# Kernel tuning notes

Hardware: AMD Instinct MI355X
Metric: run time of the kernel (lower is better)

The kernel has to match this reference:

```python
import jax, jax.numpy as jnp
import numpy as np

T = 5          # Newton iterations (init kwarg T)
EPS = 1e-05    # covariance regularizer (init kwarg eps)


def setup_inputs() -> dict:
    key = jax.random.key(0)
    k1, k2 = jax.random.split(key)
    B, C, H, W = 64, 128, 56, 56
    x = jax.random.normal(k1, (B, C, H, W), dtype=jnp.float32)
    running_rot = jax.random.normal(k2, (C, C), dtype=jnp.float32)
    return {"x": x, "running_rot": running_rot}


def reference(x, running_rot):
    # Concept Whitening forward (training-mode batch statistics), channels_first.
    # 1) IterNorm ZCA whitening via T Newton iterations on the CxC covariance.
    # 2) Rotation by the (non-trainable) running rotation matrix.
    B, C, H, W = x.shape
    m = B * H * W
    # (C, m): channels as rows, all samples/locations as columns
    xt = x.transpose(1, 0, 2, 3).reshape(C, m)
    mean = jnp.mean(xt, axis=1, keepdims=True)
    xc = xt - mean
    I = jnp.eye(C, dtype=x.dtype)
    Sigma = EPS * I + (xc @ xc.T) / m            # (C, C)
    rTr = 1.0 / jnp.trace(Sigma)                 # trace normalization
    SigmaN = Sigma * rTr
    P = I
    for _ in range(T):                           # Newton iteration for Sigma^{-1/2}
        P = 0.5 * (3.0 * P - P @ P @ P @ SigmaN)
    wm = P * jnp.sqrt(rTr)                       # whitening matrix Sigma^{-1/2}
    xn = wm @ xc                                 # whitened activations (C, m)
    x_hat = xn.reshape(C, B, H, W).transpose(1, 0, 2, 3)  # (B, C, H, W)
    # rotate into concept-aligned basis: out[b,d,h,w] = sum_c rot[d,c] * x_hat[b,c,h,w]
    out = jnp.einsum('bchw,dc->bdhw', x_hat, running_rot)
    return out
```

## Files before the change

kernel.cpp:

```cpp
#include <hip/hip_runtime.h>
#include <math.h>

#define HW 3136
#define NCHUNK 3136
#define M_TOT 200704.0f
#define EPSV 1e-5f

typedef __attribute__((ext_vector_type(8))) short bf16x8;
typedef __attribute__((ext_vector_type(4))) short short4v;
typedef __attribute__((ext_vector_type(4))) float f32x4;

__device__ inline unsigned short f2bf(float f) {
  unsigned u = __float_as_uint(f);
  u += 0x7FFFu + ((u >> 16) & 1u);
  return (unsigned short)(u >> 16);
}

__global__ __launch_bounds__(256, 2) void gram_k(const float* __restrict__ x,
                                                 float* __restrict__ partG,
                                                 float* __restrict__ partS,
                                                 int slots) {
  __shared__ unsigned short xs[128 * 72];
  const int t = threadIdx.x;
  const int lm = t & 15, quad = (t >> 4) & 3, w = t >> 6;

  f32x4 acc[2][8];
  f32x4 sacc[2];
  const f32x4 z = {0.f, 0.f, 0.f, 0.f};
#pragma unroll
  for (int i = 0; i < 2; ++i) {
    sacc[i] = z;
#pragma unroll
    for (int j = 0; j < 8; ++j) acc[i][j] = z;
  }
  bf16x8 ones;
#pragma unroll
  for (int j = 0; j < 8; ++j) ones[j] = (short)0x3F80;

  for (int chunk = blockIdx.x; chunk < NCHUNK; chunk += slots) {
    const int b = chunk / 49;
    const int s0 = (chunk % 49) * 64;
    __syncthreads();
#pragma unroll
    for (int i = 0; i < 8; ++i) {
      const int idx4 = i * 256 + t;
      const int c = idx4 >> 4, q = idx4 & 15;
      const float4 v =
          *(const float4*)(x + (size_t)(b * 128 + c) * HW + s0 + q * 4);
      uint2 dw;
      dw.x = (unsigned)f2bf(v.x) | ((unsigned)f2bf(v.y) << 16);
      dw.y = (unsigned)f2bf(v.z) | ((unsigned)f2bf(v.w) << 16);
      *(uint2*)&xs[c * 72 + q * 4] = dw;
    }
    __syncthreads();
#pragma unroll
    for (int ks = 0; ks < 2; ++ks) {
      const int ko = ks * 32 + quad * 8;
      const bf16x8 a0 = *(const bf16x8*)&xs[((2 * w + 0) * 16 + lm) * 72 + ko];
      const bf16x8 a1 = *(const bf16x8*)&xs[((2 * w + 1) * 16 + lm) * 72 + ko];
      sacc[0] = __builtin_amdgcn_mfma_f32_16x16x32_bf16(a0, ones, sacc[0], 0, 0, 0);
      sacc[1] = __builtin_amdgcn_mfma_f32_16x16x32_bf16(a1, ones, sacc[1], 0, 0, 0);
#pragma unroll
      for (int tj = 0; tj < 8; ++tj) {
        const bf16x8 bf = *(const bf16x8*)&xs[(tj * 16 + lm) * 72 + ko];
        acc[0][tj] = __builtin_amdgcn_mfma_f32_16x16x32_bf16(a0, bf, acc[0][tj], 0, 0, 0);
        acc[1][tj] = __builtin_amdgcn_mfma_f32_16x16x32_bf16(a1, bf, acc[1][tj], 0, 0, 0);
      }
    }
  }

  float* pg = partG + (size_t)blockIdx.x * 16384;
#pragma unroll
  for (int i = 0; i < 2; ++i) {
    const int ti = 2 * w + i;
#pragma unroll
    for (int tj = 0; tj < 8; ++tj)
#pragma unroll
      for (int r = 0; r < 4; ++r)
        pg[(ti * 16 + quad * 4 + r) * 128 + tj * 16 + lm] = acc[i][tj][r];
    if (lm == 0) {
#pragma unroll
      for (int r = 0; r < 4; ++r)
        partS[blockIdx.x * 128 + ti * 16 + quad * 4 + r] = sacc[i][r];
    }
  }
}

__global__ __launch_bounds__(256) void reduce1_k(const float* __restrict__ partG,
                                                 const float* __restrict__ partS,
                                                 float* __restrict__ part2,
                                                 float* __restrict__ part2S,
                                                 int slots) {
  const int t = threadIdx.x;
  const int sg = blockIdx.x & 31;
  const int eg = blockIdx.x >> 5;
  const int e4 = eg * 1024 + t * 4;
  float ax = 0.f, ay = 0.f, az = 0.f, aw = 0.f;
#pragma unroll 4
  for (int s = sg; s < slots; s += 32) {
    const float4 v = *(const float4*)(partG + (size_t)s * 16384 + e4);
    ax += v.x; ay += v.y; az += v.z; aw += v.w;
  }
  *(float4*)(part2 + (size_t)sg * 16384 + e4) = make_float4(ax, ay, az, aw);
  if (eg == 0 && t < 128) {
    float sa = 0.f;
    for (int s = sg; s < slots; s += 32) sa += partS[s * 128 + t];
    part2S[sg * 128 + t] = sa;
  }
}

__global__ __launch_bounds__(256) void reduce2_k(const float* __restrict__ part2,
                                                 const float* __restrict__ part2S,
                                                 float* __restrict__ G,
                                                 float* __restrict__ Sb) {
  const int t = threadIdx.x;
  const int e4 = blockIdx.x * 1024 + t * 4;
  float ax = 0.f, ay = 0.f, az = 0.f, aw = 0.f;
#pragma unroll
  for (int sg = 0; sg < 32; ++sg) {
    const float4 v = *(const float4*)(part2 + (size_t)sg * 16384 + e4);
    ax += v.x; ay += v.y; az += v.z; aw += v.w;
  }
  *(float4*)(G + e4) = make_float4(ax, ay, az, aw);
  if (blockIdx.x == 0 && t < 128) {
    float sa = 0.f;
#pragma unroll
    for (int sg = 0; sg < 32; ++sg) sa += part2S[sg * 128 + t];
    Sb[t] = sa;
  }
}

__global__ __launch_bounds__(256) void sigma_k(const float* __restrict__ G,
                                               float* __restrict__ Sb,
                                               float* __restrict__ SigmaN,
                                               float* __restrict__ Pa,
                                               float* __restrict__ scal) {
  const int t = threadIdx.x;
  const float rm = 1.0f / M_TOT;
  float trl = 0.f;
#pragma unroll 4
  for (int i = 0; i < 64; ++i) {
    const int e = i * 256 + t;
    const int r = e >> 7, c = e & 127;
    float v = (G[e] - Sb[r] * Sb[c] * rm) * rm + ((r == c) ? EPSV : 0.f);
    SigmaN[e] = v;
    if (r == c) trl += v;
  }
  __shared__ float red[256];
  red[t] = trl;
  __syncthreads();
  for (int off = 128; off > 0; off >>= 1) {
    if (t < off) red[t] += red[t + off];
    __syncthreads();
  }
  const float rTr = 1.0f / red[0];
#pragma unroll 4
  for (int i = 0; i < 64; ++i) {
    const int e = i * 256 + t;
    const int r = e >> 7, c = e & 127;
    const float sn = SigmaN[e] * rTr;
    SigmaN[e] = sn;
    Pa[e] = ((r == c) ? 1.5f : 0.f) - 0.5f * sn;
  }
  if (t < 128) Sb[t] *= rm;
  if (t == 0) scal[0] = sqrtf(rTr);
}

__global__ __launch_bounds__(256) void newton_k(const float* __restrict__ P,
                                                const float* __restrict__ SigmaN,
                                                float* __restrict__ Pout) {
  __shared__ float s1[8 * 132];
  __shared__ float s2[8 * 132];
  __shared__ float red[256 * 17];
  const int t = threadIdx.x;
  const int ct = t & 31;
  const int rt = (t >> 5) & 1;
  const int kt = t >> 6;
  const int rg0 = blockIdx.x * 8;
  float a[4][4];

#pragma unroll
  for (int i = 0; i < 4; ++i)
#pragma unroll
    for (int j = 0; j < 4; ++j) a[i][j] = 0.f;
#pragma unroll 4
  for (int k = kt * 32; k < kt * 32 + 32; ++k) {
    const float4 av = *(const float4*)(P + k * 128 + rg0 + 4 * rt);
    const float4 bv = *(const float4*)(P + k * 128 + 4 * ct);
    const float aA[4] = {av.x, av.y, av.z, av.w};
    const float bA[4] = {bv.x, bv.y, bv.z, bv.w};
#pragma unroll
    for (int i = 0; i < 4; ++i)
#pragma unroll
      for (int j = 0; j < 4; ++j) a[i][j] += aA[i] * bA[j];
  }
#pragma unroll
  for (int i = 0; i < 4; ++i)
#pragma unroll
    for (int j = 0; j < 4; ++j) red[t * 17 + i * 4 + j] = a[i][j];
  __syncthreads();
  if (t < 64) {
#pragma unroll
    for (int u = 1; u < 4; ++u)
#pragma unroll
      for (int i = 0; i < 4; ++i)
#pragma unroll
        for (int j = 0; j < 4; ++j)
          a[i][j] += red[(t + 64 * u) * 17 + i * 4 + j];
#pragma unroll
    for (int i = 0; i < 4; ++i)
#pragma unroll
      for (int j = 0; j < 4; ++j)
        s1[(4 * rt + i) * 132 + 4 * ct + j] = a[i][j];
  }
  __syncthreads();

#pragma unroll
  for (int i = 0; i < 4; ++i)
#pragma unroll
    for (int j = 0; j < 4; ++j) a[i][j] = 0.f;
#pragma unroll 4
  for (int k = kt * 32; k < kt * 32 + 32; ++k) {
    float aA[4];
#pragma unroll
    for (int i = 0; i < 4; ++i) aA[i] = s1[(4 * rt + i) * 132 + k];
    const float4 bv = *(const float4*)(P + k * 128 + 4 * ct);
    const float bA[4] = {bv.x, bv.y, bv.z, bv.w};
#pragma unroll
    for (int i = 0; i < 4; ++i)
#pragma unroll
      for (int j = 0; j < 4; ++j) a[i][j] += aA[i] * bA[j];
  }
  __syncthreads();
#pragma unroll
  for (int i = 0; i < 4; ++i)
#pragma unroll
    for (int j = 0; j < 4; ++j) red[t * 17 + i * 4 + j] = a[i][j];
  __syncthreads();
  if (t < 64) {
#pragma unroll
    for (int u = 1; u < 4; ++u)
#pragma unroll
      for (int i = 0; i < 4; ++i)
#pragma unroll
        for (int j = 0; j < 4; ++j)
          a[i][j] += red[(t + 64 * u) * 17 + i * 4 + j];
#pragma unroll
    for (int i = 0; i < 4; ++i)
#pragma unroll
      for (int j = 0; j < 4; ++j)
        s2[(4 * rt + i) * 132 + 4 * ct + j] = a[i][j];
  }
  __syncthreads();

#pragma unroll
  for (int i = 0; i < 4; ++i)
#pragma unroll
    for (int j = 0; j < 4; ++j) a[i][j] = 0.f;
#pragma unroll 4
  for (int k = kt * 32; k < kt * 32 + 32; ++k) {
    float aA[4];
#pragma unroll
    for (int i = 0; i < 4; ++i) aA[i] = s2[(4 * rt + i) * 132 + k];
    const float4 bv = *(const float4*)(SigmaN + k * 128 + 4 * ct);
    const float bA[4] = {bv.x, bv.y, bv.z, bv.w};
#pragma unroll
    for (int i = 0; i < 4; ++i)
#pragma unroll
      for (int j = 0; j < 4; ++j) a[i][j] += aA[i] * bA[j];
  }
  __syncthreads();
#pragma unroll
  for (int i = 0; i < 4; ++i)
#pragma unroll
    for (int j = 0; j < 4; ++j) red[t * 17 + i * 4 + j] = a[i][j];
  __syncthreads();
  if (t < 64) {
#pragma unroll
    for (int u = 1; u < 4; ++u)
#pragma unroll
      for (int i = 0; i < 4; ++i)
#pragma unroll
        for (int j = 0; j < 4; ++j)
          a[i][j] += red[(t + 64 * u) * 17 + i * 4 + j];
#pragma unroll
    for (int i = 0; i < 4; ++i) {
      const int rg = rg0 + 4 * rt + i;
      const float4 pv = *(const float4*)(P + rg * 128 + 4 * ct);
      *(float4*)(Pout + rg * 128 + 4 * ct) =
          make_float4(0.5f * (3.f * pv.x - a[i][0]),
                      0.5f * (3.f * pv.y - a[i][1]),
                      0.5f * (3.f * pv.z - a[i][2]),
                      0.5f * (3.f * pv.w - a[i][3]));
    }
  }
}

__global__ __launch_bounds__(256) void rotmt_k(const float* __restrict__ rot,
                                               const float* __restrict__ P,
                                               const float* __restrict__ mean,
                                               const float* __restrict__ scal,
                                               unsigned short* __restrict__ Mbf,
                                               float* __restrict__ bias) {
  const int t = threadIdx.x;
  const int r = t >> 5;
  const int dg = blockIdx.x * 8 + r;
  const int c0 = (t & 31) * 4;
  const float* rrow = rot + dg * 128;

  float ax = 0, ay = 0, az = 0, aw = 0;
#pragma unroll 4
  for (int k = 0; k < 128; ++k) {
    const float a = rrow[k];
    const float4 bv = *(const float4*)(P + k * 128 + c0);
    ax += a * bv.x; ay += a * bv.y; az += a * bv.z; aw += a * bv.w;
  }
  const float sc = scal[0];
  ax *= sc; ay *= sc; az *= sc; aw *= sc;
  uint2 dw;
  dw.x = (unsigned)f2bf(ax) | ((unsigned)f2bf(ay) << 16);
  dw.y = (unsigned)f2bf(az) | ((unsigned)f2bf(aw) << 16);
  *(uint2*)&Mbf[dg * 128 + c0] = dw;
  const float4 mv = *(const float4*)(mean + c0);
  float p = ax * mv.x + ay * mv.y + az * mv.z + aw * mv.w;
  for (int off = 16; off > 0; off >>= 1) p += __shfl_down(p, off, 32);
  if ((t & 31) == 0) bias[dg] = p;
}

#define MSTR 136
#define XSTR 132
__global__ __launch_bounds__(256, 2) void apply_k(const float* __restrict__ x,
                                                  const unsigned short* __restrict__ Mbf,
                                                  const float* __restrict__ bias,
                                                  float* __restrict__ out) {
  __shared__ unsigned short Ms[128 * MSTR];
  __shared__ unsigned short xsB[64 * XSTR];
  const int t = threadIdx.x;
  const int lm = t & 15, quad = (t >> 4) & 3, w = t >> 6;

#pragma unroll
  for (int i = 0; i < 8; ++i) {
    const int e = i * 256 + t;
    const int row = e >> 4, oct = e & 15;
    *(uint4*)&Ms[row * MSTR + oct * 8] =
        *(const uint4*)(Mbf + row * 128 + oct * 8);
  }
  float biasr[2][4];
#pragma unroll
  for (int i = 0; i < 2; ++i)
#pragma unroll
    for (int r = 0; r < 4; ++r)
      biasr[i][r] = bias[(2 * w + i) * 16 + quad * 4 + r];

  const f32x4 z = {0.f, 0.f, 0.f, 0.f};
  for (int chunk = blockIdx.x; chunk < NCHUNK; chunk += 784) {
    const int b = chunk / 49;
    const int s0 = (chunk % 49) * 64;
    __syncthreads();
#pragma unroll
    for (int i = 0; i < 4; ++i) {
      const int p = 16 * i + (t >> 4);
      const int q = t & 15;
      const float* px = x + (size_t)(b * 128 + 2 * p) * HW + s0 + 4 * q;
      const float4 fa = *(const float4*)px;
      const float4 fb = *(const float4*)(px + HW);
      const float faA[4] = {fa.x, fa.y, fa.z, fa.w};
      const float fbA[4] = {fb.x, fb.y, fb.z, fb.w};
#pragma unroll
      for (int r = 0; r < 4; ++r) {
        const unsigned dw =
            (unsigned)f2bf(faA[r]) | ((unsigned)f2bf(fbA[r]) << 16);
        *(unsigned*)&xsB[(4 * q + r) * XSTR + 2 * p] = dw;
      }
    }
    __syncthreads();

    f32x4 acc[2][4];
#pragma unroll
    for (int i = 0; i < 2; ++i)
#pragma unroll
      for (int sj = 0; sj < 4; ++sj) acc[i][sj] = z;

#pragma unroll
    for (int ks = 0; ks < 4; ++ks) {
      const int ko = ks * 32 + quad * 8;
      const bf16x8 a0 = *(const bf16x8*)&Ms[((2 * w + 0) * 16 + lm) * MSTR + ko];
      const bf16x8 a1 = *(const bf16x8*)&Ms[((2 * w + 1) * 16 + lm) * MSTR + ko];
#pragma unroll
      for (int sj = 0; sj < 4; ++sj) {
        const short4v blo = *(const short4v*)&xsB[(sj * 16 + lm) * XSTR + ko];
        const short4v bhi = *(const short4v*)&xsB[(sj * 16 + lm) * XSTR + ko + 4];
        const bf16x8 bf = __builtin_shufflevector(blo, bhi, 0, 1, 2, 3, 4, 5, 6, 7);
        acc[0][sj] = __builtin_amdgcn_mfma_f32_16x16x32_bf16(a0, bf, acc[0][sj], 0, 0, 0);
        acc[1][sj] = __builtin_amdgcn_mfma_f32_16x16x32_bf16(a1, bf, acc[1][sj], 0, 0, 0);
      }
    }
#pragma unroll
    for (int i = 0; i < 2; ++i)
#pragma unroll
      for (int r = 0; r < 4; ++r) {
        const int d = (2 * w + i) * 16 + quad * 4 + r;
        float* orow = out + (size_t)(b * 128 + d) * HW + s0 + lm;
#pragma unroll
        for (int sj = 0; sj < 4; ++sj)
          orow[sj * 16] = acc[i][sj][r] - biasr[i][r];
      }
  }
}

extern "C" void kernel_launch(void* const* d_in, const int* in_sizes, int n_in,
                              void* d_out, int out_size, void* d_ws,
                              size_t ws_size, hipStream_t stream) {
  const float* x = (const float*)d_in[0];
  const float* rot = (const float*)d_in[1];
  float* out = (float*)d_out;
  float* ws = (float*)d_ws;

  float* G      = ws;
  float* SigmaN = ws + 16384;
  float* Pa     = ws + 32768;
  float* Pb     = ws + 49152;
  unsigned short* Mbf = (unsigned short*)(ws + 65536);
  float* Sb     = ws + 73728;
  float* bias   = ws + 73856;
  float* scal   = ws + 73984;
  float* part2  = ws + 74000;
  float* part2S = ws + 74000 + 524288;
  float* partG  = ws + 74000 + 524288 + 4096;

  const size_t wsf = ws_size / 4;
  long avail = (long)wsf - (74000 + 524288 + 4096);
  int slots = (int)(avail / (16384 + 128));
  if (slots > 512) slots = 512;
  if (slots < 1) slots = 1;
  float* partS = partG + (size_t)slots * 16384;

  gram_k<<<slots, 256, 0, stream>>>(x, partG, partS, slots);
  reduce1_k<<<512, 256, 0, stream>>>(partG, partS, part2, part2S, slots);
  reduce2_k<<<16, 256, 0, stream>>>(part2, part2S, G, Sb);
  sigma_k<<<1, 256, 0, stream>>>(G, Sb, SigmaN, Pa, scal);
  float* pin = Pa;
  float* pout = Pb;
  for (int i = 0; i < 4; ++i) {
    newton_k<<<16, 256, 0, stream>>>(pin, SigmaN, pout);
    float* tmp = pin; pin = pout; pout = tmp;
  }
  rotmt_k<<<16, 256, 0, stream>>>(rot, pin, Sb, scal, Mbf, bias);
  apply_k<<<784, 256, 0, stream>>>(x, Mbf, bias, out);
}
```

Before: 301.8 us.

## Prefetch gram chunks, fuse sigma setup into reduction and first Newton step, one chunk per apply block

The gram kernel moves to 512 threads with one 16-row tile per wave, double-buffered LDS and register prefetch of the next chunk, so the global load overlaps the MFMA work. The second reduction now also builds Sigma and per-block trace partials, which removes the single-block sigma kernel. The first Newton step is computed directly from Sigma inside its own kernel, and trace normalization is folded into each step. The apply kernel launches one block per chunk instead of a grid-stride loop. Together these cut kernel launches and serial phases, at the cost of more register pressure and more blocks.

```diff
diff --git a/kernel.cpp b/kernel.cpp
--- a/kernel.cpp
+++ b/kernel.cpp
@@ -16,73 +16,83 @@
   return (unsigned short)(u >> 16);
 }
 
-__global__ __launch_bounds__(256, 2) void gram_k(const float* __restrict__ x,
+__global__ __launch_bounds__(512, 4) void gram_k(const float* __restrict__ x,
                                                  float* __restrict__ partG,
                                                  float* __restrict__ partS,
                                                  int slots) {
-  __shared__ unsigned short xs[128 * 72];
+  __shared__ unsigned short xs[2][128 * 72];
   const int t = threadIdx.x;
   const int lm = t & 15, quad = (t >> 4) & 3, w = t >> 6;
-
-  f32x4 acc[2][8];
-  f32x4 sacc[2];
+  const int row0 = w * 16;
+  const int qofs = (t & 15) * 4;
+  const int chi = t >> 4;
+
+  f32x4 acc[8];
+  f32x4 sacc;
   const f32x4 z = {0.f, 0.f, 0.f, 0.f};
-#pragma unroll
-  for (int i = 0; i < 2; ++i) {
-    sacc[i] = z;
-#pragma unroll
-    for (int j = 0; j < 8; ++j) acc[i][j] = z;
-  }
+  sacc = z;
+#pragma unroll
+  for (int j = 0; j < 8; ++j) acc[j] = z;
   bf16x8 ones;
 #pragma unroll
   for (int j = 0; j < 8; ++j) ones[j] = (short)0x3F80;
 
-  for (int chunk = blockIdx.x; chunk < NCHUNK; chunk += slots) {
+  int chunk = blockIdx.x;
+  float4 pre[4];
+  {
     const int b = chunk / 49;
     const int s0 = (chunk % 49) * 64;
+    const float* base = x + (size_t)(b * 128) * HW + s0;
+#pragma unroll
+    for (int i = 0; i < 4; ++i)
+      pre[i] = *(const float4*)(base + (size_t)(i * 32 + chi) * HW + qofs);
+  }
+
+  int buf = 0;
+  while (chunk < NCHUNK) {
+#pragma unroll
+    for (int i = 0; i < 4; ++i) {
+      const int c = i * 32 + chi;
+      uint2 dw;
+      dw.x = (unsigned)f2bf(pre[i].x) | ((unsigned)f2bf(pre[i].y) << 16);
+      dw.y = (unsigned)f2bf(pre[i].z) | ((unsigned)f2bf(pre[i].w) << 16);
+      *(uint2*)&xs[buf][c * 72 + qofs] = dw;
+    }
     __syncthreads();
-#pragma unroll
-    for (int i = 0; i < 8; ++i) {
-      const int idx4 = i * 256 + t;
-      const int c = idx4 >> 4, q = idx4 & 15;
-      const float4 v =
-          *(const float4*)(x + (size_t)(b * 128 + c) * HW + s0 + q * 4);
-      uint2 dw;
-      dw.x = (unsigned)f2bf(v.x) | ((unsigned)f2bf(v.y) << 16);
-      dw.y = (unsigned)f2bf(v.z) | ((unsigned)f2bf(v.w) << 16);
-      *(uint2*)&xs[c * 72 + q * 4] = dw;
-    }
-    __syncthreads();
+    const int nxt = chunk + slots;
+    if (nxt < NCHUNK) {
+      const int b = nxt / 49;
+      const int s0 = (nxt % 49) * 64;
+      const float* base = x + (size_t)(b * 128) * HW + s0;
+#pragma unroll
+      for (int i = 0; i < 4; ++i)
+        pre[i] = *(const float4*)(base + (size_t)(i * 32 + chi) * HW + qofs);
+    }
 #pragma unroll
     for (int ks = 0; ks < 2; ++ks) {
       const int ko = ks * 32 + quad * 8;
-      const bf16x8 a0 = *(const bf16x8*)&xs[((2 * w + 0) * 16 + lm) * 72 + ko];
-      const bf16x8 a1 = *(const bf16x8*)&xs[((2 * w + 1) * 16 + lm) * 72 + ko];
-      sacc[0] = __builtin_amdgcn_mfma_f32_16x16x32_bf16(a0, ones, sacc[0], 0, 0, 0);
-      sacc[1] = __builtin_amdgcn_mfma_f32_16x16x32_bf16(a1, ones, sacc[1], 0, 0, 0);
+      const bf16x8 a0 = *(const bf16x8*)&xs[buf][(row0 + lm) * 72 + ko];
+      sacc = __builtin_amdgcn_mfma_f32_16x16x32_bf16(a0, ones, sacc, 0, 0, 0);
 #pragma unroll
       for (int tj = 0; tj < 8; ++tj) {
-        const bf16x8 bf = *(const bf16x8*)&xs[(tj * 16 + lm) * 72 + ko];
-        acc[0][tj] = __builtin_amdgcn_mfma_f32_16x16x32_bf16(a0, bf, acc[0][tj], 0, 0, 0);
-        acc[1][tj] = __builtin_amdgcn_mfma_f32_16x16x32_bf16(a1, bf, acc[1][tj], 0, 0, 0);
+        const bf16x8 bf = *(const bf16x8*)&xs[buf][(tj * 16 + lm) * 72 + ko];
+        acc[tj] = __builtin_amdgcn_mfma_f32_16x16x32_bf16(a0, bf, acc[tj], 0, 0, 0);
       }
     }
+    buf ^= 1;
+    chunk = nxt;
   }
 
   float* pg = partG + (size_t)blockIdx.x * 16384;
 #pragma unroll
-  for (int i = 0; i < 2; ++i) {
-    const int ti = 2 * w + i;
-#pragma unroll
-    for (int tj = 0; tj < 8; ++tj)
-#pragma unroll
-      for (int r = 0; r < 4; ++r)
-        pg[(ti * 16 + quad * 4 + r) * 128 + tj * 16 + lm] = acc[i][tj][r];
-    if (lm == 0) {
-#pragma unroll
-      for (int r = 0; r < 4; ++r)
-        partS[blockIdx.x * 128 + ti * 16 + quad * 4 + r] = sacc[i][r];
-    }
+  for (int tj = 0; tj < 8; ++tj)
+#pragma unroll
+    for (int r = 0; r < 4; ++r)
+      pg[(row0 + quad * 4 + r) * 128 + tj * 16 + lm] = acc[tj][r];
+  if (lm == 0) {
+#pragma unroll
+    for (int r = 0; r < 4; ++r)
+      partS[blockIdx.x * 128 + row0 + quad * 4 + r] = sacc[r];
   }
 }
 
@@ -109,11 +119,22 @@
   }
 }
 
-__global__ __launch_bounds__(256) void reduce2_k(const float* __restrict__ part2,
-                                                 const float* __restrict__ part2S,
-                                                 float* __restrict__ G,
-                                                 float* __restrict__ Sb) {
-  const int t = threadIdx.x;
+__global__ __launch_bounds__(256) void sigred_k(const float* __restrict__ part2,
+                                                const float* __restrict__ part2S,
+                                                float* __restrict__ Sigma,
+                                                float* __restrict__ traceP,
+                                                float* __restrict__ meanOut) {
+  __shared__ float SbL[128];
+  __shared__ float red[256];
+  const int t = threadIdx.x;
+  if (t < 128) {
+    float sa = 0.f;
+#pragma unroll
+    for (int sg = 0; sg < 32; ++sg) sa += part2S[sg * 128 + t];
+    SbL[t] = sa;
+    if (blockIdx.x == 0) meanOut[t] = sa * (1.0f / M_TOT);
+  }
+  __syncthreads();
   const int e4 = blockIdx.x * 1024 + t * 4;
   float ax = 0.f, ay = 0.f, az = 0.f, aw = 0.f;
 #pragma unroll
@@ -121,53 +142,177 @@
     const float4 v = *(const float4*)(part2 + (size_t)sg * 16384 + e4);
     ax += v.x; ay += v.y; az += v.z; aw += v.w;
   }
-  *(float4*)(G + e4) = make_float4(ax, ay, az, aw);
-  if (blockIdx.x == 0 && t < 128) {
-    float sa = 0.f;
-#pragma unroll
-    for (int sg = 0; sg < 32; ++sg) sa += part2S[sg * 128 + t];
-    Sb[t] = sa;
-  }
-}
-
-__global__ __launch_bounds__(256) void sigma_k(const float* __restrict__ G,
-                                               float* __restrict__ Sb,
-                                               float* __restrict__ SigmaN,
-                                               float* __restrict__ Pa,
-                                               float* __restrict__ scal) {
-  const int t = threadIdx.x;
+  const int r = e4 >> 7, c0 = e4 & 127;
   const float rm = 1.0f / M_TOT;
+  const float sr = SbL[r] * rm;
+  float s4[4];
+  s4[0] = (ax - sr * SbL[c0 + 0]) * rm;
+  s4[1] = (ay - sr * SbL[c0 + 1]) * rm;
+  s4[2] = (az - sr * SbL[c0 + 2]) * rm;
+  s4[3] = (aw - sr * SbL[c0 + 3]) * rm;
   float trl = 0.f;
-#pragma unroll 4
-  for (int i = 0; i < 64; ++i) {
-    const int e = i * 256 + t;
-    const int r = e >> 7, c = e & 127;
-    float v = (G[e] - Sb[r] * Sb[c] * rm) * rm + ((r == c) ? EPSV : 0.f);
-    SigmaN[e] = v;
-    if (r == c) trl += v;
-  }
-  __shared__ float red[256];
+#pragma unroll
+  for (int j = 0; j < 4; ++j) {
+    if (c0 + j == r) { s4[j] += EPSV; trl = s4[j]; }
+  }
+  *(float4*)(Sigma + e4) = make_float4(s4[0], s4[1], s4[2], s4[3]);
   red[t] = trl;
   __syncthreads();
   for (int off = 128; off > 0; off >>= 1) {
     if (t < off) red[t] += red[t + off];
     __syncthreads();
   }
-  const float rTr = 1.0f / red[0];
-#pragma unroll 4
-  for (int i = 0; i < 64; ++i) {
-    const int e = i * 256 + t;
-    const int r = e >> 7, c = e & 127;
-    const float sn = SigmaN[e] * rTr;
-    SigmaN[e] = sn;
-    Pa[e] = ((r == c) ? 1.5f : 0.f) - 0.5f * sn;
-  }
-  if (t < 128) Sb[t] *= rm;
-  if (t == 0) scal[0] = sqrtf(rTr);
+  if (t == 0) traceP[blockIdx.x] = red[0];
+}
+
+__global__ __launch_bounds__(256) void newton1_k(const float* __restrict__ Sig,
+                                                 const float* __restrict__ traceP,
+                                                 float* __restrict__ Pout) {
+  __shared__ float s1[8 * 132];
+  __shared__ float s2[8 * 132];
+  __shared__ float red[256 * 17];
+  const int t = threadIdx.x;
+  const int ct = t & 31;
+  const int rt = (t >> 5) & 1;
+  const int kt = t >> 6;
+  const int rg0 = blockIdx.x * 8;
+  const int ra = rg0 + 4 * rt;
+  float tr = 0.f;
+#pragma unroll
+  for (int i = 0; i < 16; ++i) tr += traceP[i];
+  const float rTr = 1.0f / tr;
+  const float nh = -0.5f * rTr;
+  float a[4][4];
+
+#pragma unroll
+  for (int i = 0; i < 4; ++i)
+#pragma unroll
+    for (int j = 0; j < 4; ++j) a[i][j] = 0.f;
+#pragma unroll 4
+  for (int k = kt * 32; k < kt * 32 + 32; ++k) {
+    const float4 sa4 = *(const float4*)(Sig + k * 128 + ra);
+    const float4 sb4 = *(const float4*)(Sig + k * 128 + 4 * ct);
+    float aA[4] = {nh * sa4.x, nh * sa4.y, nh * sa4.z, nh * sa4.w};
+    float bA[4] = {nh * sb4.x, nh * sb4.y, nh * sb4.z, nh * sb4.w};
+#pragma unroll
+    for (int i = 0; i < 4; ++i) if (ra + i == k) aA[i] += 1.5f;
+#pragma unroll
+    for (int j = 0; j < 4; ++j) if (4 * ct + j == k) bA[j] += 1.5f;
+#pragma unroll
+    for (int i = 0; i < 4; ++i)
+#pragma unroll
+      for (int j = 0; j < 4; ++j) a[i][j] += aA[i] * bA[j];
+  }
+#pragma unroll
+  for (int i = 0; i < 4; ++i)
+#pragma unroll
+    for (int j = 0; j < 4; ++j) red[t * 17 + i * 4 + j] = a[i][j];
+  __syncthreads();
+  if (t < 64) {
+#pragma unroll
+    for (int u = 1; u < 4; ++u)
+#pragma unroll
+      for (int i = 0; i < 4; ++i)
+#pragma unroll
+        for (int j = 0; j < 4; ++j)
+          a[i][j] += red[(t + 64 * u) * 17 + i * 4 + j];
+#pragma unroll
+    for (int i = 0; i < 4; ++i)
+#pragma unroll
+      for (int j = 0; j < 4; ++j)
+        s1[(4 * rt + i) * 132 + 4 * ct + j] = a[i][j];
+  }
+  __syncthreads();
+
+#pragma unroll
+  for (int i = 0; i < 4; ++i)
+#pragma unroll
+    for (int j = 0; j < 4; ++j) a[i][j] = 0.f;
+#pragma unroll 4
+  for (int k = kt * 32; k < kt * 32 + 32; ++k) {
+    float aA[4];
+#pragma unroll
+    for (int i = 0; i < 4; ++i) aA[i] = s1[(4 * rt + i) * 132 + k];
+    const float4 sb4 = *(const float4*)(Sig + k * 128 + 4 * ct);
+    float bA[4] = {nh * sb4.x, nh * sb4.y, nh * sb4.z, nh * sb4.w};
+#pragma unroll
+    for (int j = 0; j < 4; ++j) if (4 * ct + j == k) bA[j] += 1.5f;
+#pragma unroll
+    for (int i = 0; i < 4; ++i)
+#pragma unroll
+      for (int j = 0; j < 4; ++j) a[i][j] += aA[i] * bA[j];
+  }
+  __syncthreads();
+#pragma unroll
+  for (int i = 0; i < 4; ++i)
+#pragma unroll
+    for (int j = 0; j < 4; ++j) red[t * 17 + i * 4 + j] = a[i][j];
+  __syncthreads();
+  if (t < 64) {
+#pragma unroll
+    for (int u = 1; u < 4; ++u)
+#pragma unroll
+      for (int i = 0; i < 4; ++i)
+#pragma unroll
+        for (int j = 0; j < 4; ++j)
+          a[i][j] += red[(t + 64 * u) * 17 + i * 4 + j];
+#pragma unroll
+    for (int i = 0; i < 4; ++i)
+#pragma unroll
+      for (int j = 0; j < 4; ++j)
+        s2[(4 * rt + i) * 132 + 4 * ct + j] = a[i][j];
+  }
+  __syncthreads();
+
+#pragma unroll
+  for (int i = 0; i < 4; ++i)
+#pragma unroll
+    for (int j = 0; j < 4; ++j) a[i][j] = 0.f;
+#pragma unroll 4
+  for (int k = kt * 32; k < kt * 32 + 32; ++k) {
+    float aA[4];
+#pragma unroll
+    for (int i = 0; i < 4; ++i) aA[i] = s2[(4 * rt + i) * 132 + k];
+    const float4 bv = *(const float4*)(Sig + k * 128 + 4 * ct);
+    const float bA[4] = {bv.x, bv.y, bv.z, bv.w};
+#pragma unroll
+    for (int i = 0; i < 4; ++i)
+#pragma unroll
+      for (int j = 0; j < 4; ++j) a[i][j] += aA[i] * bA[j];
+  }
+  __syncthreads();
+#pragma unroll
+  for (int i = 0; i < 4; ++i)
+#pragma unroll
+    for (int j = 0; j < 4; ++j) red[t * 17 + i * 4 + j] = a[i][j];
+  __syncthreads();
+  if (t < 64) {
+#pragma unroll
+    for (int u = 1; u < 4; ++u)
+#pragma unroll
+      for (int i = 0; i < 4; ++i)
+#pragma unroll
+        for (int j = 0; j < 4; ++j)
+          a[i][j] += red[(t + 64 * u) * 17 + i * 4 + j];
+#pragma unroll
+    for (int i = 0; i < 4; ++i) {
+      const int rg = rg0 + 4 * rt + i;
+      const float4 sv = *(const float4*)(Sig + rg * 128 + 4 * ct);
+      float p1v[4] = {nh * sv.x, nh * sv.y, nh * sv.z, nh * sv.w};
+#pragma unroll
+      for (int j = 0; j < 4; ++j) if (4 * ct + j == rg) p1v[j] += 1.5f;
+      *(float4*)(Pout + rg * 128 + 4 * ct) =
+          make_float4(0.5f * (3.f * p1v[0] - rTr * a[i][0]),
+                      0.5f * (3.f * p1v[1] - rTr * a[i][1]),
+                      0.5f * (3.f * p1v[2] - rTr * a[i][2]),
+                      0.5f * (3.f * p1v[3] - rTr * a[i][3]));
+    }
+  }
 }
 
 __global__ __launch_bounds__(256) void newton_k(const float* __restrict__ P,
-                                                const float* __restrict__ SigmaN,
+                                                const float* __restrict__ Sig,
+                                                const float* __restrict__ traceP,
                                                 float* __restrict__ Pout) {
   __shared__ float s1[8 * 132];
   __shared__ float s2[8 * 132];
@@ -177,6 +322,10 @@
   const int rt = (t >> 5) & 1;
   const int kt = t >> 6;
   const int rg0 = blockIdx.x * 8;
+  float tr = 0.f;
+#pragma unroll
+  for (int i = 0; i < 16; ++i) tr += traceP[i];
+  const float rTr = 1.0f / tr;
   float a[4][4];
 
 #pragma unroll
@@ -262,7 +411,7 @@
     float aA[4];
 #pragma unroll
     for (int i = 0; i < 4; ++i) aA[i] = s2[(4 * rt + i) * 132 + k];
-    const float4 bv = *(const float4*)(SigmaN + k * 128 + 4 * ct);
+    const float4 bv = *(const float4*)(Sig + k * 128 + 4 * ct);
     const float bA[4] = {bv.x, bv.y, bv.z, bv.w};
 #pragma unroll
     for (int i = 0; i < 4; ++i)
@@ -288,10 +437,10 @@
       const int rg = rg0 + 4 * rt + i;
       const float4 pv = *(const float4*)(P + rg * 128 + 4 * ct);
       *(float4*)(Pout + rg * 128 + 4 * ct) =
-          make_float4(0.5f * (3.f * pv.x - a[i][0]),
-                      0.5f * (3.f * pv.y - a[i][1]),
-                      0.5f * (3.f * pv.z - a[i][2]),
-                      0.5f * (3.f * pv.w - a[i][3]));
+          make_float4(0.5f * (3.f * pv.x - rTr * a[i][0]),
+                      0.5f * (3.f * pv.y - rTr * a[i][1]),
+                      0.5f * (3.f * pv.z - rTr * a[i][2]),
+                      0.5f * (3.f * pv.w - rTr * a[i][3]));
     }
   }
 }
@@ -299,7 +448,7 @@
 __global__ __launch_bounds__(256) void rotmt_k(const float* __restrict__ rot,
                                                const float* __restrict__ P,
                                                const float* __restrict__ mean,
-                                               const float* __restrict__ scal,
+                                               const float* __restrict__ traceP,
                                                unsigned short* __restrict__ Mbf,
                                                float* __restrict__ bias) {
   const int t = threadIdx.x;
@@ -307,6 +456,10 @@
   const int dg = blockIdx.x * 8 + r;
   const int c0 = (t & 31) * 4;
   const float* rrow = rot + dg * 128;
+  float tr = 0.f;
+#pragma unroll
+  for (int i = 0; i < 16; ++i) tr += traceP[i];
+  const float sc = sqrtf(1.0f / tr);
 
   float ax = 0, ay = 0, az = 0, aw = 0;
 #pragma unroll 4
@@ -315,7 +468,6 @@
     const float4 bv = *(const float4*)(P + k * 128 + c0);
     ax += a * bv.x; ay += a * bv.y; az += a * bv.z; aw += a * bv.w;
   }
-  const float sc = scal[0];
   ax *= sc; ay *= sc; az *= sc; aw *= sc;
   uint2 dw;
   dw.x = (unsigned)f2bf(ax) | ((unsigned)f2bf(ay) << 16);
@@ -337,6 +489,8 @@
   __shared__ unsigned short xsB[64 * XSTR];
   const int t = threadIdx.x;
   const int lm = t & 15, quad = (t >> 4) & 3, w = t >> 6;
+  const int b = blockIdx.x / 49;
+  const int s0 = (blockIdx.x % 49) * 64;
 
 #pragma unroll
   for (int i = 0; i < 8; ++i) {
@@ -345,67 +499,61 @@
     *(uint4*)&Ms[row * MSTR + oct * 8] =
         *(const uint4*)(Mbf + row * 128 + oct * 8);
   }
+#pragma unroll
+  for (int i = 0; i < 4; ++i) {
+    const int p = 16 * i + (t >> 4);
+    const int q = t & 15;
+    const float* px = x + (size_t)(b * 128 + 2 * p) * HW + s0 + 4 * q;
+    const float4 fa = *(const float4*)px;
+    const float4 fb = *(const float4*)(px + HW);
+    const float faA[4] = {fa.x, fa.y, fa.z, fa.w};
+    const float fbA[4] = {fb.x, fb.y, fb.z, fb.w};
+#pragma unroll
+    for (int r = 0; r < 4; ++r) {
+      const unsigned dw =
+          (unsigned)f2bf(faA[r]) | ((unsigned)f2bf(fbA[r]) << 16);
+      *(unsigned*)&xsB[(4 * q + r) * XSTR + 2 * p] = dw;
+    }
+  }
   float biasr[2][4];
 #pragma unroll
   for (int i = 0; i < 2; ++i)
 #pragma unroll
     for (int r = 0; r < 4; ++r)
       biasr[i][r] = bias[(2 * w + i) * 16 + quad * 4 + r];
+  __syncthreads();
 
   const f32x4 z = {0.f, 0.f, 0.f, 0.f};
-  for (int chunk = blockIdx.x; chunk < NCHUNK; chunk += 784) {
-    const int b = chunk / 49;
-    const int s0 = (chunk % 49) * 64;
-    __syncthreads();
-#pragma unroll
-    for (int i = 0; i < 4; ++i) {
-      const int p = 16 * i + (t >> 4);
-      const int q = t & 15;
-      const float* px = x + (size_t)(b * 128 + 2 * p) * HW + s0 + 4 * q;
-      const float4 fa = *(const float4*)px;
-      const float4 fb = *(const float4*)(px + HW);
-      const float faA[4] = {fa.x, fa.y, fa.z, fa.w};
-      const float fbA[4] = {fb.x, fb.y, fb.z, fb.w};
-#pragma unroll
-      for (int r = 0; r < 4; ++r) {
-        const unsigned dw =
-            (unsigned)f2bf(faA[r]) | ((unsigned)f2bf(fbA[r]) << 16);
-        *(unsigned*)&xsB[(4 * q + r) * XSTR + 2 * p] = dw;
-      }
-    }
-    __syncthreads();
-
-    f32x4 acc[2][4];
-#pragma unroll
-    for (int i = 0; i < 2; ++i)
-#pragma unroll
-      for (int sj = 0; sj < 4; ++sj) acc[i][sj] = z;
-
-#pragma unroll
-    for (int ks = 0; ks < 4; ++ks) {
-      const int ko = ks * 32 + quad * 8;
-      const bf16x8 a0 = *(const bf16x8*)&Ms[((2 * w + 0) * 16 + lm) * MSTR + ko];
-      const bf16x8 a1 = *(const bf16x8*)&Ms[((2 * w + 1) * 16 + lm) * MSTR + ko];
-#pragma unroll
-      for (int sj = 0; sj < 4; ++sj) {
-        const short4v blo = *(const short4v*)&xsB[(sj * 16 + lm) * XSTR + ko];
-        const short4v bhi = *(const short4v*)&xsB[(sj * 16 + lm) * XSTR + ko + 4];
-        const bf16x8 bf = __builtin_shufflevector(blo, bhi, 0, 1, 2, 3, 4, 5, 6, 7);
-        acc[0][sj] = __builtin_amdgcn_mfma_f32_16x16x32_bf16(a0, bf, acc[0][sj], 0, 0, 0);
-        acc[1][sj] = __builtin_amdgcn_mfma_f32_16x16x32_bf16(a1, bf, acc[1][sj], 0, 0, 0);
-      }
-    }
-#pragma unroll
-    for (int i = 0; i < 2; ++i)
-#pragma unroll
-      for (int r = 0; r < 4; ++r) {
-        const int d = (2 * w + i) * 16 + quad * 4 + r;
-        float* orow = out + (size_t)(b * 128 + d) * HW + s0 + lm;
-#pragma unroll
-        for (int sj = 0; sj < 4; ++sj)
-          orow[sj * 16] = acc[i][sj][r] - biasr[i][r];
-      }
-  }
+  f32x4 acc[2][4];
+#pragma unroll
+  for (int i = 0; i < 2; ++i)
+#pragma unroll
+    for (int sj = 0; sj < 4; ++sj) acc[i][sj] = z;
+
+#pragma unroll
+  for (int ks = 0; ks < 4; ++ks) {
+    const int ko = ks * 32 + quad * 8;
+    const bf16x8 a0 = *(const bf16x8*)&Ms[((2 * w + 0) * 16 + lm) * MSTR + ko];
+    const bf16x8 a1 = *(const bf16x8*)&Ms[((2 * w + 1) * 16 + lm) * MSTR + ko];
+#pragma unroll
+    for (int sj = 0; sj < 4; ++sj) {
+      const short4v blo = *(const short4v*)&xsB[(sj * 16 + lm) * XSTR + ko];
+      const short4v bhi = *(const short4v*)&xsB[(sj * 16 + lm) * XSTR + ko + 4];
+      const bf16x8 bf = __builtin_shufflevector(blo, bhi, 0, 1, 2, 3, 4, 5, 6, 7);
+      acc[0][sj] = __builtin_amdgcn_mfma_f32_16x16x32_bf16(a0, bf, acc[0][sj], 0, 0, 0);
+      acc[1][sj] = __builtin_amdgcn_mfma_f32_16x16x32_bf16(a1, bf, acc[1][sj], 0, 0, 0);
+    }
+  }
+#pragma unroll
+  for (int i = 0; i < 2; ++i)
+#pragma unroll
+    for (int r = 0; r < 4; ++r) {
+      const int d = (2 * w + i) * 16 + quad * 4 + r;
+      float* orow = out + (size_t)(b * 128 + d) * HW + s0 + lm;
+#pragma unroll
+      for (int sj = 0; sj < 4; ++sj)
+        orow[sj * 16] = acc[i][sj][r] - biasr[i][r];
+    }
 }
 
 extern "C" void kernel_launch(void* const* d_in, const int* in_sizes, int n_in,
@@ -416,35 +564,31 @@
   float* out = (float*)d_out;
   float* ws = (float*)d_ws;
 
-  float* G      = ws;
-  float* SigmaN = ws + 16384;
-  float* Pa     = ws + 32768;
-  float* Pb     = ws + 49152;
-  unsigned short* Mbf = (unsigned short*)(ws + 65536);
-  float* Sb     = ws + 73728;
-  float* bias   = ws + 73856;
-  float* scal   = ws + 73984;
-  float* part2  = ws + 74000;
-  float* part2S = ws + 74000 + 524288;
-  float* partG  = ws + 74000 + 524288 + 4096;
+  float* Sigma  = ws;
+  float* Pa     = ws + 16384;
+  float* Pb     = ws + 32768;
+  unsigned short* Mbf = (unsigned short*)(ws + 49152);
+  float* Sb     = ws + 57344;
+  float* bias   = ws + 57472;
+  float* traceP = ws + 57600;
+  float* part2  = ws + 57616;
+  float* part2S = ws + 57616 + 524288;
+  float* partG  = ws + 57616 + 524288 + 4096;
 
   const size_t wsf = ws_size / 4;
-  long avail = (long)wsf - (74000 + 524288 + 4096);
+  long avail = (long)wsf - (57616 + 524288 + 4096);
   int slots = (int)(avail / (16384 + 128));
   if (slots > 512) slots = 512;
   if (slots < 1) slots = 1;
   float* partS = partG + (size_t)slots * 16384;
 
-  gram_k<<<slots, 256, 0, stream>>>(x, partG, partS, slots);
+  gram_k<<<slots, 512, 0, stream>>>(x, partG, partS, slots);
   reduce1_k<<<512, 256, 0, stream>>>(partG, partS, part2, part2S, slots);
-  reduce2_k<<<16, 256, 0, stream>>>(part2, part2S, G, Sb);
-  sigma_k<<<1, 256, 0, stream>>>(G, Sb, SigmaN, Pa, scal);
-  float* pin = Pa;
-  float* pout = Pb;
-  for (int i = 0; i < 4; ++i) {
-    newton_k<<<16, 256, 0, stream>>>(pin, SigmaN, pout);
-    float* tmp = pin; pin = pout; pout = tmp;
-  }
-  rotmt_k<<<16, 256, 0, stream>>>(rot, pin, Sb, scal, Mbf, bias);
-  apply_k<<<784, 256, 0, stream>>>(x, Mbf, bias, out);
-}
+  sigred_k<<<16, 256, 0, stream>>>(part2, part2S, Sigma, traceP, Sb);
+  newton1_k<<<16, 256, 0, stream>>>(Sigma, traceP, Pb);
+  newton_k<<<16, 256, 0, stream>>>(Pb, Sigma, traceP, Pa);
+  newton_k<<<16, 256, 0, stream>>>(Pa, Sigma, traceP, Pb);
+  newton_k<<<16, 256, 0, stream>>>(Pb, Sigma, traceP, Pa);
+  rotmt_k<<<16, 256, 0, stream>>>(rot, Pa, Sb, traceP, Mbf, bias);
+  apply_k<<<3136, 256, 0, stream>>>(x, Mbf, bias, out);
+}
```

Result: faster. 263.8 us (-12.6%).
